# Optimization experiments

Hardware: AMD Instinct MI355X
Metric: run time of the kernel (lower is better)

## Reference

```python
import jax, jax.numpy as jnp
import numpy as np

N, G, F, H, P, OUT = 100000, 64, 64, 128, 2, 2
E = 1_600_000
BN_EPS = 1e-5  # PyG BatchNorm eps; eval mode with running_mean=0, running_var=1


def setup_inputs() -> dict:
    key = jax.random.key(0)
    ks = iter(jax.random.split(key, 64))

    def lin(din, dout):
        w = jax.random.normal(next(ks), (din, dout), jnp.float32) / np.sqrt(din).astype(np.float32)
        return w, jnp.zeros((dout,), jnp.float32)

    inp = {}
    inp["x"] = jax.random.normal(next(ks), (N, F), jnp.float32)
    inp["pos"] = jax.random.normal(next(ks), (N, P), jnp.float32)
    inp["edge_index"] = jax.random.randint(next(ks), (2, E), 0, N, dtype=jnp.int64) if jax.config.jax_enable_x64 else jax.random.randint(next(ks), (2, E), 0, N)
    inp["batch"] = jnp.sort(jax.random.randint(next(ks), (N,), 0, G))
    dims = [F + P, H + P, H + P]
    for l, din in enumerate(dims):
        w1, b1 = lin(din, H)
        w2, b2 = lin(H, H)
        inp[f"w{l}1"], inp[f"b{l}1"] = w1, b1
        inp[f"g{l}1"], inp[f"be{l}1"] = jnp.ones((H,), jnp.float32), jnp.zeros((H,), jnp.float32)
        inp[f"w{l}2"], inp[f"b{l}2"] = w2, b2
        inp[f"g{l}2"], inp[f"be{l}2"] = jnp.ones((H,), jnp.float32), jnp.zeros((H,), jnp.float32)
    inp["wlin"], inp["blin"] = lin(H, OUT)
    return inp


def _bn(h, g, b):
    # eval-mode BatchNorm with running_mean=0, running_var=1
    return h * (g * (1.0 / np.sqrt(1.0 + BN_EPS)).astype(np.float32)) + b


def _mlp(h, w1, b1, g1, be1, w2, b2, g2, be2):
    h = jax.nn.relu(_bn(h @ w1 + b1, g1, be1))
    return jax.nn.relu(_bn(h @ w2 + b2, g2, be2))


def _gin_max(x, src, dst, mlp_params):
    # GINConv with aggr='max', eps=0: mlp(x + max_{j in N(i)} x_j), empty neighborhoods -> 0 (PyG scatter fill)
    agg = jax.ops.segment_max(x[src], dst, num_segments=N)  # [N, C]
    agg = jnp.where(jnp.isneginf(agg), jnp.zeros((), agg.dtype), agg)
    return _mlp(x + agg, *mlp_params)


def reference(x, pos, edge_index, batch,
              w01, b01, g01, be01, w02, b02, g02, be02,
              w11, b11, g11, be11, w12, b12, g12, be12,
              w21, b21, g21, be21, w22, b22, g22, be22,
              wlin, blin):
    src, dst = edge_index[0], edge_index[1]
    h = jnp.concatenate([x, pos], axis=-1)                        # [N, F+P]
    h = _gin_max(h, src, dst, (w01, b01, g01, be01, w02, b02, g02, be02))
    h = jnp.concatenate([h, pos], axis=-1)                        # [N, H+P]
    h = _gin_max(h, src, dst, (w11, b11, g11, be11, w12, b12, g12, be12))
    h = jnp.concatenate([h, pos], axis=-1)
    h = _gin_max(h, src, dst, (w21, b21, g21, be21, w22, b22, g22, be22))
    pooled = jax.ops.segment_max(h, batch, num_segments=G)        # global_max_pool -> [G, H]
    pooled = jnp.where(jnp.isneginf(pooled), jnp.zeros((), pooled.dtype), pooled)
    return pooled @ wlin + blin                                   # logits [G, OUT]
```

## Files before the change

### kernel.cpp

```cpp
#include <hip/hip_runtime.h>
#include <hip/hip_fp16.h>
#include <math.h>
#include <string.h>

constexpr int HDIM = 128;
constexpr int ZR   = 160;
constexpr int ZS   = 168;
constexpr float BN_INV = 0.99999500003749980f;

typedef _Float16 half8v __attribute__((ext_vector_type(8)));
typedef __attribute__((ext_vector_type(4))) float float4v;

__device__ __forceinline__ unsigned pkmax(unsigned a, unsigned b) {
  unsigned r;
  asm volatile("v_pk_max_f16 %0, %1, %2" : "=v"(r) : "v"(a), "v"(b));
  return r;
}
__device__ __forceinline__ unsigned pkadd(unsigned a, unsigned b) {
  unsigned r;
  asm volatile("v_pk_add_f16 %0, %1, %2" : "=v"(r) : "v"(a), "v"(b));
  return r;
}

__device__ __forceinline__ float us2f(unsigned short u) { __half h; memcpy(&h, &u, 2); return __half2float(h); }
__device__ __forceinline__ unsigned short f2us(float f) {
  __half h = __float2half(f); unsigned short u; memcpy(&u, &h, 2); return u;
}

__device__ __forceinline__ unsigned encf(float f) {
  unsigned u = __float_as_uint(f);
  return (u & 0x80000000u) ? ~u : (u | 0x80000000u);
}
__device__ __forceinline__ float decf(unsigned u) {
  return (u & 0x80000000u) ? __uint_as_float(u ^ 0x80000000u) : __uint_as_float(~u);
}

__global__ __launch_bounds__(256) void k_bcnt(
    const int* __restrict__ ei, int* __restrict__ bcnt, int E, int shift, int nbkt) {
  __shared__ int hb[256];
  const int tid = threadIdx.x;
  hb[tid] = 0;
  __syncthreads();
  const int base = blockIdx.x * 4096;
#pragma unroll
  for (int k = 0; k < 16; ++k) {
    int e = base + k * 256 + tid;
    if (e < E) atomicAdd(&hb[ei[E + e] >> shift], 1);
  }
  __syncthreads();
  if (tid < nbkt && hb[tid] > 0) atomicAdd(&bcnt[tid], hb[tid]);
}

__global__ __launch_bounds__(256) void k_bscan(
    const int* __restrict__ bcnt, int* __restrict__ bbase, int* __restrict__ gcur,
    int nbkt, int E) {
  __shared__ int s[256];
  int tid = threadIdx.x;
  int v = (tid < nbkt) ? bcnt[tid] : 0;
  s[tid] = v;
  __syncthreads();
  for (int off = 1; off < 256; off <<= 1) {
    int t = (tid >= off) ? s[tid - off] : 0;
    __syncthreads();
    s[tid] += t;
    __syncthreads();
  }
  if (tid < nbkt) {
    int e = s[tid] - v;
    bbase[tid] = e;
    gcur[tid] = e;
  }
  if (tid == 0) bbase[nbkt] = E;
}

__global__ __launch_bounds__(256) void k_bscatter(
    const int* __restrict__ ei, int* __restrict__ gcur,
    unsigned long long* __restrict__ sorted, int E, int shift, int nbkt) {
  __shared__ int hcnt[256];
  __shared__ int hstart[256];
  __shared__ int gbase[256];
  __shared__ unsigned long long sbuf[4096];

  const int tid = threadIdx.x;
  const int base = blockIdx.x * 4096;
  const int validCount = min(4096, E - base);

  hcnt[tid] = 0;
  __syncthreads();

  int sArr[16], dArr[16];
#pragma unroll
  for (int k = 0; k < 16; ++k) {
    int e = base + k * 256 + tid;
    if (e < E) {
      sArr[k] = ei[e];
      dArr[k] = ei[E + e];
      atomicAdd(&hcnt[dArr[k] >> shift], 1);
    } else {
      sArr[k] = -1; dArr[k] = -1;
    }
  }
  __syncthreads();

  {
    int v = hcnt[tid];
    __shared__ int sc[256];
    sc[tid] = v;
    __syncthreads();
    for (int off = 1; off < 256; off <<= 1) {
      int t = (tid >= off) ? sc[tid - off] : 0;
      __syncthreads();
      sc[tid] += t;
      __syncthreads();
    }
    hstart[tid] = sc[tid] - v;
    if (tid < nbkt && v > 0) gbase[tid] = atomicAdd(&gcur[tid], v);
    hcnt[tid] = sc[tid] - v;
  }
  __syncthreads();

#pragma unroll
  for (int k = 0; k < 16; ++k) {
    if (dArr[k] >= 0) {
      int b = dArr[k] >> shift;
      int p = atomicAdd(&hcnt[b], 1);
      sbuf[p] = ((unsigned long long)(unsigned)dArr[k] << 32) | (unsigned)sArr[k];
    }
  }
  __syncthreads();

  for (int p = tid; p < validCount; p += 256) {
    unsigned long long v = sbuf[p];
    int b = (int)(v >> 32) >> shift;
    sorted[(size_t)gbase[b] + (p - hstart[b])] = v;
  }
}

__global__ __launch_bounds__(256) void k_bcsr(
    const unsigned long long* __restrict__ sorted, const int* __restrict__ bbase,
    int* __restrict__ rowptr, int* __restrict__ eidx,
    int shift, int nbkt, int N, int E) {
  __shared__ int cnt[512];
  __shared__ int excl[512];
  __shared__ int sc[256];
  const int b = blockIdx.x, tid = threadIdx.x;
  const int nodeBase = b << shift;
  const int nodesHere = min(512, N - nodeBase);
  const int lo = bbase[b], hi = bbase[b + 1];

  cnt[tid] = 0; cnt[tid + 256] = 0;
  __syncthreads();
  for (int i = lo + tid; i < hi; i += 256) {
    int d = (int)(sorted[i] >> 32);
    atomicAdd(&cnt[d - nodeBase], 1);
  }
  __syncthreads();
  int a0 = cnt[2 * tid], a1 = cnt[2 * tid + 1];
  int pv = a0 + a1;
  sc[tid] = pv;
  __syncthreads();
  for (int off = 1; off < 256; off <<= 1) {
    int t = (tid >= off) ? sc[tid - off] : 0;
    __syncthreads();
    sc[tid] += t;
    __syncthreads();
  }
  int pe = sc[tid] - pv;
  excl[2 * tid] = pe;
  excl[2 * tid + 1] = pe + a0;
  __syncthreads();
  for (int i = tid; i < 512; i += 256) {
    if (i < nodesHere) rowptr[nodeBase + i] = lo + excl[i];
    cnt[i] = excl[i];
  }
  if (b == nbkt - 1 && tid == 0) rowptr[N] = E;
  __syncthreads();
  for (int i = lo + tid; i < hi; i += 256) {
    unsigned long long v = sorted[i];
    int d = (int)(v >> 32);
    int s = (int)(v & 0xFFFFFFFFu);
    int p = atomicAdd(&cnt[d - nodeBase], 1);
    eidx[lo + p] = s;
  }
}

struct PrepArgs {
  const float *x, *pos;
  const float *w01, *w11, *w21, *w02, *w12, *w22;
  const float *b01, *g01, *e01, *b02, *g02, *e02;
  const float *b11, *g11, *e11, *b12, *g12, *e12;
  const float *b21, *g21, *e21, *b22, *g22, *e22;
  unsigned short *h0;
  unsigned *posq;
  unsigned short *Wt;
  unsigned *pooled;
  float *Ep;
  int N, GH;
};

__global__ __launch_bounds__(256) void k_prep(PrepArgs a) {
  const int gtid = blockIdx.x * 256 + threadIdx.x;

  if (gtid < a.GH) a.pooled[gtid] = 0x007FFFFFu;

  if (gtid < 61440) {
    int l = gtid / 20480, rem = gtid % 20480;
    int n = rem / 160, k = rem % 160;
    const float* W = (l == 0) ? a.w01 : ((l == 1) ? a.w11 : a.w21);
    int K = (l == 0) ? 66 : 130;
    float v = (k < K) ? W[(size_t)k * 128 + n] : 0.0f;
    a.Wt[gtid] = f2us(v);
  } else if (gtid < 110592) {
    int idx2 = gtid - 61440;
    int l = idx2 / 16384, rem = idx2 % 16384;
    int n = rem / 128, k = rem % 128;
    const float* W = (l == 0) ? a.w02 : ((l == 1) ? a.w12 : a.w22);
    a.Wt[gtid] = f2us(W[(size_t)k * 128 + n]);
  } else if (gtid < 110592 + 768) {
    int idx = gtid - 110592;
    int col = idx & 127, stage = (idx >> 7) & 1, l = idx >> 8;
    const float *bb, *gg, *ee;
    if (l == 0)      { if (!stage) { bb = a.b01; gg = a.g01; ee = a.e01; } else { bb = a.b02; gg = a.g02; ee = a.e02; } }
    else if (l == 1) { if (!stage) { bb = a.b11; gg = a.g11; ee = a.e11; } else { bb = a.b12; gg = a.g12; ee = a.e12; } }
    else             { if (!stage) { bb = a.b21; gg = a.g21; ee = a.e21; } else { bb = a.b22; gg = a.g22; ee = a.e22; } }
    float s = gg[col] * BN_INV;
    a.Ep[l * 512 + stage * 256 + col] = s;
    a.Ep[l * 512 + stage * 256 + 128 + col] = bb[col] * s + ee[col];
  }

  int r = gtid >> 6;
  if (r < a.N) {
    int lane = gtid & 63;
    a.h0[(size_t)r * HDIM + lane] = f2us(a.x[(size_t)r * 64 + lane]);
    float pv = (lane < 2) ? a.pos[(size_t)r * 2 + lane] : 0.0f;
    a.h0[(size_t)r * HDIM + 64 + lane] = f2us(pv);
    if (lane == 0) {
      unsigned p2 = (unsigned)f2us(a.pos[(size_t)r * 2]) |
                    ((unsigned)f2us(a.pos[(size_t)r * 2 + 1]) << 16);
      a.posq[r] = p2;
    }
  }
}

__global__ __launch_bounds__(256) void k_agg(
    const unsigned short* __restrict__ hcat, const unsigned* __restrict__ posq,
    const int* __restrict__ rowptr, const int* __restrict__ eidx,
    unsigned short* __restrict__ z, int actA, int doTail, int N) {
  int wid = (int)((blockIdx.x * 256 + threadIdx.x) >> 6);
  if (wid >= N) return;
  const int lane = threadIdx.x & 63;
  const int half = lane >> 5;
  const int lc = lane & 31;
  const bool act = lc < actA;
  const bool tail = doTail && (lc == 16);
  const int cb = lc * 8;

  const unsigned NEGINF = 0xFC00FC00u;
  unsigned m0 = NEGINF, m1 = NEGINF, m2 = NEGINF, m3 = NEGINF, mt = NEGINF;

  int r0 = rowptr[wid], r1 = rowptr[wid + 1];
  int e = r0 + half;
  for (; e + 6 < r1; e += 8) {
    int s0 = eidx[e], s1 = eidx[e + 2], s2 = eidx[e + 4], s3 = eidx[e + 6];
    if (act) {
      uint4 v0 = *(const uint4*)(hcat + (size_t)s0 * HDIM + cb);
      uint4 v1 = *(const uint4*)(hcat + (size_t)s1 * HDIM + cb);
      uint4 v2 = *(const uint4*)(hcat + (size_t)s2 * HDIM + cb);
      uint4 v3 = *(const uint4*)(hcat + (size_t)s3 * HDIM + cb);
      m0 = pkmax(m0, pkmax(pkmax(v0.x, v1.x), pkmax(v2.x, v3.x)));
      m1 = pkmax(m1, pkmax(pkmax(v0.y, v1.y), pkmax(v2.y, v3.y)));
      m2 = pkmax(m2, pkmax(pkmax(v0.z, v1.z), pkmax(v2.z, v3.z)));
      m3 = pkmax(m3, pkmax(pkmax(v0.w, v1.w), pkmax(v2.w, v3.w)));
    }
    if (tail) {
      mt = pkmax(mt, pkmax(pkmax(posq[s0], posq[s1]), pkmax(posq[s2], posq[s3])));
    }
  }
  for (; e < r1; e += 2) {
    int s = eidx[e];
    if (act) {
      uint4 va = *(const uint4*)(hcat + (size_t)s * HDIM + cb);
      m0 = pkmax(m0, va.x);
      m1 = pkmax(m1, va.y);
      m2 = pkmax(m2, va.z);
      m3 = pkmax(m3, va.w);
    }
    if (tail) mt = pkmax(mt, posq[s]);
  }

  m0 = pkmax(m0, (unsigned)__shfl_xor((int)m0, 32));
  m1 = pkmax(m1, (unsigned)__shfl_xor((int)m1, 32));
  m2 = pkmax(m2, (unsigned)__shfl_xor((int)m2, 32));
  m3 = pkmax(m3, (unsigned)__shfl_xor((int)m3, 32));
  mt = pkmax(mt, (unsigned)__shfl_xor((int)mt, 32));

  if (half == 0) {
    const bool none = (r0 == r1);
    if (act) {
      if (none) { m0 = 0u; m1 = 0u; m2 = 0u; m3 = 0u; }
      uint4 sv = *(const uint4*)(hcat + (size_t)wid * HDIM + cb);
      uint4 o;
      o.x = pkadd(sv.x, m0);
      o.y = pkadd(sv.y, m1);
      o.z = pkadd(sv.z, m2);
      o.w = pkadd(sv.w, m3);
      *(uint4*)(z + (size_t)wid * ZR + cb) = o;
    }
    if (tail) {
      if (none) mt = 0u;
      *(unsigned*)(z + (size_t)wid * ZR + 128) = pkadd(posq[wid], mt);
    }
  }
}

__global__ __launch_bounds__(256) void k_mlp(
    const unsigned short* __restrict__ z, int kc1,
    const unsigned short* __restrict__ Wt1, const float* __restrict__ Ep1,
    const unsigned short* __restrict__ Wt2, const float* __restrict__ Ep2,
    unsigned short* __restrict__ out, int N) {
  __shared__ __align__(16) unsigned short zs[4][16][ZS];
  const int tid = threadIdx.x;
  const int w = tid >> 6, lane = tid & 63;
  const int arow = lane & 15;
  const int grp  = lane >> 4;
  const int row0 = blockIdx.x * 64 + w * 16;

  for (int c = lane; c < 16 * 20; c += 64) {
    int r = c / 20, seg = c - r * 20;
    int gr = row0 + r;
    if (gr >= N) gr = N - 1;
    uint4 v = *(const uint4*)(z + (size_t)gr * ZR + seg * 8);
    *(uint4*)(&zs[w][r][seg * 8]) = v;
  }

  float4v acc[8];
#pragma unroll
  for (int i = 0; i < 8; ++i) acc[i] = (float4v){0.f, 0.f, 0.f, 0.f};

  for (int kc = 0; kc < kc1; ++kc) {
    half8v a = *(const half8v*)(&zs[w][arow][kc * 32 + grp * 8]);
    const unsigned short* wp = Wt1 + (size_t)arow * 160 + kc * 32 + grp * 8;
#pragma unroll
    for (int nt = 0; nt < 8; ++nt) {
      half8v b = *(const half8v*)(wp + (size_t)(nt * 16) * 160);
      acc[nt] = __builtin_amdgcn_mfma_f32_16x16x32_f16(a, b, acc[nt], 0, 0, 0);
    }
  }

#pragma unroll
  for (int nt = 0; nt < 8; ++nt) {
    int col = nt * 16 + arow;
    float sc = Ep1[col];
    float cc = Ep1[128 + col];
#pragma unroll
    for (int j = 0; j < 4; ++j) {
      float v = fmaxf(fmaf(acc[nt][j], sc, cc), 0.0f);
      zs[w][grp * 4 + j][col] = f2us(v);
    }
  }

#pragma unroll
  for (int i = 0; i < 8; ++i) acc[i] = (float4v){0.f, 0.f, 0.f, 0.f};
  for (int kc = 0; kc < 4; ++kc) {
    half8v a = *(const half8v*)(&zs[w][arow][kc * 32 + grp * 8]);
    const unsigned short* wp = Wt2 + (size_t)arow * HDIM + kc * 32 + grp * 8;
#pragma unroll
    for (int nt = 0; nt < 8; ++nt) {
      half8v b = *(const half8v*)(wp + (size_t)(nt * 16) * HDIM);
      acc[nt] = __builtin_amdgcn_mfma_f32_16x16x32_f16(a, b, acc[nt], 0, 0, 0);
    }
  }

#pragma unroll
  for (int nt = 0; nt < 8; ++nt) {
    int col = nt * 16 + arow;
    float sc = Ep2[col];
    float cc = Ep2[128 + col];
#pragma unroll
    for (int j = 0; j < 4; ++j) {
      int gr = row0 + grp * 4 + j;
      if (gr < N) {
        float v = fmaxf(fmaf(acc[nt][j], sc, cc), 0.0f);
        out[(size_t)gr * HDIM + col] = f2us(v);
      }
    }
  }
}

__global__ __launch_bounds__(128) void k_pool(
    const unsigned short* __restrict__ hcat, const int* __restrict__ batch,
    unsigned* __restrict__ pooled, int N) {
  int base = blockIdx.x * 128;
  int c = threadIdx.x;
  int end = min(base + 128, N);
  int curg = -1;
  float m = -INFINITY;
  for (int i = base; i < end; ++i) {
    int g = batch[i];
    if (g != curg) {
      if (curg >= 0) atomicMax(&pooled[curg * HDIM + c], encf(m));
      curg = g;
      m = -INFINITY;
    }
    m = fmaxf(m, us2f(hcat[(size_t)i * HDIM + c]));
  }
  if (curg >= 0) atomicMax(&pooled[curg * HDIM + c], encf(m));
}

__global__ __launch_bounds__(64) void k_final(
    const unsigned* __restrict__ pooled, const float* __restrict__ wlin,
    const float* __restrict__ blin, float* __restrict__ out) {
  int g = blockIdx.x;
  int lane = threadIdx.x;
  float v0 = decf(pooled[g * HDIM + lane]);
  float v1 = decf(pooled[g * HDIM + 64 + lane]);
  if (v0 == -INFINITY) v0 = 0.0f;
  if (v1 == -INFINITY) v1 = 0.0f;
  float p0 = v0 * wlin[lane * 2 + 0] + v1 * wlin[(64 + lane) * 2 + 0];
  float p1 = v0 * wlin[lane * 2 + 1] + v1 * wlin[(64 + lane) * 2 + 1];
  for (int off = 32; off > 0; off >>= 1) {
    p0 += __shfl_down(p0, off);
    p1 += __shfl_down(p1, off);
  }
  if (lane == 0) {
    out[g * 2 + 0] = p0 + blin[0];
    out[g * 2 + 1] = p1 + blin[1];
  }
}

static inline size_t ws_align(size_t x) { return (x + 511) & ~(size_t)511; }

extern "C" void kernel_launch(void* const* d_in, const int* in_sizes, int n_in,
                              void* d_out, int out_size, void* d_ws, size_t ws_size,
                              hipStream_t stream) {
  const float* x     = (const float*)d_in[0];
  const float* pos   = (const float*)d_in[1];
  const int*   ei    = (const int*)d_in[2];
  const int*   batch = (const int*)d_in[3];
  const float* wlin  = (const float*)d_in[28];
  const float* blin  = (const float*)d_in[29];

  const int N = in_sizes[3];
  const int E = in_sizes[2] / 2;
  const int G = out_size / 2;

  int shift = 9;
  while ((((N - 1) >> shift) + 1) > 256) ++shift;
  const int nbkt = ((N - 1) >> shift) + 1;
  const int chunks = (E + 4095) / 4096;

  char* w = (char*)d_ws;
  size_t off = 0;
  auto take = [&](size_t bytes) { void* p = w + off; off += ws_align(bytes); return p; };
  int*            rowptr = (int*)take((size_t)(N + 1) * 4);
  int*            bcnt   = (int*)take(1024);
  int*            bbase  = (int*)take(2048);
  int*            gcur   = (int*)take(1024);
  int*            eidx   = (int*)take((size_t)E * 4);
  unsigned long long* sorted = (unsigned long long*)take((size_t)E * 8);
  unsigned short* hcat   = (unsigned short*)take((size_t)N * HDIM * 2);
  unsigned*       posq   = (unsigned*)take((size_t)N * 4);
  unsigned short* z      = (unsigned short*)take((size_t)N * ZR * 2);
  unsigned short* Wt     = (unsigned short*)take((size_t)110592 * 2);
  float*          Ep     = (float*)take(3 * 2 * 2 * 128 * 4);
  unsigned*       pooled = (unsigned*)take((size_t)G * HDIM * 4);
  (void)ws_size;

  hipMemsetAsync(bcnt, 0, 1024, stream);
  k_bcnt<<<chunks, 256, 0, stream>>>(ei, bcnt, E, shift, nbkt);
  k_bscan<<<1, 256, 0, stream>>>(bcnt, bbase, gcur, nbkt, E);
  k_bscatter<<<chunks, 256, 0, stream>>>(ei, gcur, sorted, E, shift, nbkt);
  k_bcsr<<<nbkt, 256, 0, stream>>>(sorted, bbase, rowptr, eidx, shift, nbkt, N, E);

  {
    PrepArgs a;
    a.x = x; a.pos = pos;
    a.w01 = (const float*)d_in[4];  a.w11 = (const float*)d_in[12]; a.w21 = (const float*)d_in[20];
    a.w02 = (const float*)d_in[8];  a.w12 = (const float*)d_in[16]; a.w22 = (const float*)d_in[24];
    a.b01 = (const float*)d_in[5];  a.g01 = (const float*)d_in[6];  a.e01 = (const float*)d_in[7];
    a.b02 = (const float*)d_in[9];  a.g02 = (const float*)d_in[10]; a.e02 = (const float*)d_in[11];
    a.b11 = (const float*)d_in[13]; a.g11 = (const float*)d_in[14]; a.e11 = (const float*)d_in[15];
    a.b12 = (const float*)d_in[17]; a.g12 = (const float*)d_in[18]; a.e12 = (const float*)d_in[19];
    a.b21 = (const float*)d_in[21]; a.g21 = (const float*)d_in[22]; a.e21 = (const float*)d_in[23];
    a.b22 = (const float*)d_in[25]; a.g22 = (const float*)d_in[26]; a.e22 = (const float*)d_in[27];
    a.h0 = hcat; a.posq = posq; a.Wt = Wt; a.pooled = pooled; a.Ep = Ep;
    a.N = N; a.GH = G * HDIM;
    k_prep<<<(N + 3) / 4, 256, 0, stream>>>(a);
  }

  const int actA[3]   = {9, 16, 16};
  const int doTail[3] = {0, 1, 0};
  const int kc1a[3]   = {3, 5, 5};
  const int aggBlocks = (N + 3) / 4;
  const int mlpBlocks = (N + 63) / 64;

  for (int l = 0; l < 3; ++l) {
    const unsigned short* Wt1 = Wt + (size_t)l * 20480;
    const unsigned short* Wt2 = Wt + 61440 + (size_t)l * 16384;
    const float* Ep1 = Ep + l * 512;
    const float* Ep2 = Ep + l * 512 + 256;

    k_agg<<<aggBlocks, 256, 0, stream>>>(hcat, posq, rowptr, eidx, z,
                                         actA[l], doTail[l], N);
    k_mlp<<<mlpBlocks, 256, 0, stream>>>(z, kc1a[l], Wt1, Ep1, Wt2, Ep2, hcat, N);
  }

  k_pool<<<(N + 127) / 128, 128, 0, stream>>>(hcat, batch, pooled, N);
  k_final<<<G, 64, 0, stream>>>(pooled, wlin, blin, (float*)d_out);
}
```

Before: 518.6 us.

## Pad node feature rows to 160 halves and trim layer-0 z staging

Changes the hcat row stride from 128 to 160 halves, so gathered rows in the aggregation kernel and the MLP output writes use a padded stride, probably to move rows off power-of-two address strides and spread them across memory channels. It also lets the MLP kernel stage only the z segments each layer needs (12 for layer 0 instead of 20), and skips the tail shuffle when no tail is processed. The cost is a 25% larger hcat buffer with a looser gather footprint in cache.

```diff
diff --git a/kernel.cpp b/kernel.cpp
--- a/kernel.cpp
+++ b/kernel.cpp
@@ -4,6 +4,7 @@
 #include <string.h>
 
 constexpr int HDIM = 128;
+constexpr int HS   = 160;
 constexpr int ZR   = 160;
 constexpr int ZS   = 168;
 constexpr float BN_INV = 0.99999500003749980f;
@@ -231,9 +232,9 @@
   int r = gtid >> 6;
   if (r < a.N) {
     int lane = gtid & 63;
-    a.h0[(size_t)r * HDIM + lane] = f2us(a.x[(size_t)r * 64 + lane]);
+    a.h0[(size_t)r * HS + lane] = f2us(a.x[(size_t)r * 64 + lane]);
     float pv = (lane < 2) ? a.pos[(size_t)r * 2 + lane] : 0.0f;
-    a.h0[(size_t)r * HDIM + 64 + lane] = f2us(pv);
+    a.h0[(size_t)r * HS + 64 + lane] = f2us(pv);
     if (lane == 0) {
       unsigned p2 = (unsigned)f2us(a.pos[(size_t)r * 2]) |
                     ((unsigned)f2us(a.pos[(size_t)r * 2 + 1]) << 16);
@@ -263,10 +264,10 @@
   for (; e + 6 < r1; e += 8) {
     int s0 = eidx[e], s1 = eidx[e + 2], s2 = eidx[e + 4], s3 = eidx[e + 6];
     if (act) {
-      uint4 v0 = *(const uint4*)(hcat + (size_t)s0 * HDIM + cb);
-      uint4 v1 = *(const uint4*)(hcat + (size_t)s1 * HDIM + cb);
-      uint4 v2 = *(const uint4*)(hcat + (size_t)s2 * HDIM + cb);
-      uint4 v3 = *(const uint4*)(hcat + (size_t)s3 * HDIM + cb);
+      uint4 v0 = *(const uint4*)(hcat + (size_t)s0 * HS + cb);
+      uint4 v1 = *(const uint4*)(hcat + (size_t)s1 * HS + cb);
+      uint4 v2 = *(const uint4*)(hcat + (size_t)s2 * HS + cb);
+      uint4 v3 = *(const uint4*)(hcat + (size_t)s3 * HS + cb);
       m0 = pkmax(m0, pkmax(pkmax(v0.x, v1.x), pkmax(v2.x, v3.x)));
       m1 = pkmax(m1, pkmax(pkmax(v0.y, v1.y), pkmax(v2.y, v3.y)));
       m2 = pkmax(m2, pkmax(pkmax(v0.z, v1.z), pkmax(v2.z, v3.z)));
@@ -279,7 +280,7 @@
   for (; e < r1; e += 2) {
     int s = eidx[e];
     if (act) {
-      uint4 va = *(const uint4*)(hcat + (size_t)s * HDIM + cb);
+      uint4 va = *(const uint4*)(hcat + (size_t)s * HS + cb);
       m0 = pkmax(m0, va.x);
       m1 = pkmax(m1, va.y);
       m2 = pkmax(m2, va.z);
@@ -292,13 +293,13 @@
   m1 = pkmax(m1, (unsigned)__shfl_xor((int)m1, 32));
   m2 = pkmax(m2, (unsigned)__shfl_xor((int)m2, 32));
   m3 = pkmax(m3, (unsigned)__shfl_xor((int)m3, 32));
-  mt = pkmax(mt, (unsigned)__shfl_xor((int)mt, 32));
+  if (doTail) mt = pkmax(mt, (unsigned)__shfl_xor((int)mt, 32));
 
   if (half == 0) {
     const bool none = (r0 == r1);
     if (act) {
       if (none) { m0 = 0u; m1 = 0u; m2 = 0u; m3 = 0u; }
-      uint4 sv = *(const uint4*)(hcat + (size_t)wid * HDIM + cb);
+      uint4 sv = *(const uint4*)(hcat + (size_t)wid * HS + cb);
       uint4 o;
       o.x = pkadd(sv.x, m0);
       o.y = pkadd(sv.y, m1);
@@ -314,7 +315,7 @@
 }
 
 __global__ __launch_bounds__(256) void k_mlp(
-    const unsigned short* __restrict__ z, int kc1,
+    const unsigned short* __restrict__ z, int kc1, int nseg,
     const unsigned short* __restrict__ Wt1, const float* __restrict__ Ep1,
     const unsigned short* __restrict__ Wt2, const float* __restrict__ Ep2,
     unsigned short* __restrict__ out, int N) {
@@ -325,8 +326,8 @@
   const int grp  = lane >> 4;
   const int row0 = blockIdx.x * 64 + w * 16;
 
-  for (int c = lane; c < 16 * 20; c += 64) {
-    int r = c / 20, seg = c - r * 20;
+  for (int c = lane; c < 16 * nseg; c += 64) {
+    int r = c / nseg, seg = c - r * nseg;
     int gr = row0 + r;
     if (gr >= N) gr = N - 1;
     uint4 v = *(const uint4*)(z + (size_t)gr * ZR + seg * 8);
@@ -381,7 +382,7 @@
       int gr = row0 + grp * 4 + j;
       if (gr < N) {
         float v = fmaxf(fmaf(acc[nt][j], sc, cc), 0.0f);
-        out[(size_t)gr * HDIM + col] = f2us(v);
+        out[(size_t)gr * HS + col] = f2us(v);
       }
     }
   }
@@ -402,7 +403,7 @@
       curg = g;
       m = -INFINITY;
     }
-    m = fmaxf(m, us2f(hcat[(size_t)i * HDIM + c]));
+    m = fmaxf(m, us2f(hcat[(size_t)i * HS + c]));
   }
   if (curg >= 0) atomicMax(&pooled[curg * HDIM + c], encf(m));
 }
@@ -458,7 +459,7 @@
   int*            gcur   = (int*)take(1024);
   int*            eidx   = (int*)take((size_t)E * 4);
   unsigned long long* sorted = (unsigned long long*)take((size_t)E * 8);
-  unsigned short* hcat   = (unsigned short*)take((size_t)N * HDIM * 2);
+  unsigned short* hcat   = (unsigned short*)take((size_t)N * HS * 2);
   unsigned*       posq   = (unsigned*)take((size_t)N * 4);
   unsigned short* z      = (unsigned short*)take((size_t)N * ZR * 2);
   unsigned short* Wt     = (unsigned short*)take((size_t)110592 * 2);
@@ -491,6 +492,7 @@
   const int actA[3]   = {9, 16, 16};
   const int doTail[3] = {0, 1, 0};
   const int kc1a[3]   = {3, 5, 5};
+  const int nsega[3]  = {12, 20, 20};
   const int aggBlocks = (N + 3) / 4;
   const int mlpBlocks = (N + 63) / 64;
 
@@ -502,7 +504,8 @@
 
     k_agg<<<aggBlocks, 256, 0, stream>>>(hcat, posq, rowptr, eidx, z,
                                          actA[l], doTail[l], N);
-    k_mlp<<<mlpBlocks, 256, 0, stream>>>(z, kc1a[l], Wt1, Ep1, Wt2, Ep2, hcat, N);
+    k_mlp<<<mlpBlocks, 256, 0, stream>>>(z, kc1a[l], nsega[l], Wt1, Ep1,
+                                         Wt2, Ep2, hcat, N);
   }
 
   k_pool<<<(N + 127) / 128, 128, 0, stream>>>(hcat, batch, pooled, N);
```

After: 522.7 us. No clear change (+0.8%).
